# Optimization experiments

Measured on AMD Instinct MI355X. Metric: run time of the kernel, lower is better.

Reference implementation:

```python
import jax, jax.numpy as jnp
import numpy as np

B, H, W, C = 8, 128, 128, 192
HEADS, WS, SS = 6, 8, 4
MLP_H = 384  # mlp_ratio=2.0
N = WS * WS
NW = (H // WS) * (W // WS)


def _rel_index():
    coords = np.stack(np.meshgrid(np.arange(WS), np.arange(WS), indexing='ij'))  # [2,ws,ws]
    flat = coords.reshape(2, -1)
    rel = (flat[:, :, None] - flat[:, None, :]).transpose(1, 2, 0).astype(np.int64)  # [n,n,2]
    rel[..., 0] += WS - 1
    rel[..., 1] += WS - 1
    rel[..., 0] *= 2 * WS - 1
    return rel.sum(-1)  # [n,n]


def _attn_mask():
    img = np.zeros((H, W), dtype=np.float32)
    sl = (slice(0, -WS), slice(-WS, -SS), slice(-SS, None))
    cnt = 0
    for hs in sl:
        for ws_ in sl:
            img[hs, ws_] = cnt
            cnt += 1
    mw = img.reshape(H // WS, WS, W // WS, WS).transpose(0, 2, 1, 3).reshape(-1, N)
    diff = mw[:, None, :] - mw[:, :, None]  # [nW,n,n]
    return np.where(diff != 0, np.float32(-100.0), np.float32(0.0))


def setup_inputs() -> dict:
    key = jax.random.key(0)
    ks = jax.random.split(key, 6)
    rn = lambda k, shp: jax.random.normal(k, shp, jnp.float32) * 0.02
    return {
        'x': jax.random.normal(ks[0], (B, H * W, C), jnp.float32),
        'norm1_g': jnp.ones((C,), jnp.float32), 'norm1_b': jnp.zeros((C,), jnp.float32),
        'qkv_w': rn(ks[1], (3 * C, C)), 'qkv_b': jnp.zeros((3 * C,), jnp.float32),
        'rpb_table': rn(ks[2], ((2 * WS - 1) ** 2, HEADS)),
        'proj_w': rn(ks[3], (C, C)), 'proj_b': jnp.zeros((C,), jnp.float32),
        'norm2_g': jnp.ones((C,), jnp.float32), 'norm2_b': jnp.zeros((C,), jnp.float32),
        'fc1_w': rn(ks[4], (MLP_H, C)), 'fc1_b': jnp.zeros((MLP_H,), jnp.float32),
        'fc2_w': rn(ks[5], (C, MLP_H)), 'fc2_b': jnp.zeros((C,), jnp.float32),
        'rel_idx': jnp.asarray(_rel_index(), jnp.int32),
        'attn_mask': jnp.asarray(_attn_mask()),
    }


def _ln(x, g, b):
    m = x.mean(-1, keepdims=True)
    v = x.var(-1, keepdims=True)
    return (x - m) * jax.lax.rsqrt(v + 1e-5) * g + b


def _block(x, norm1_g, norm1_b, qkv_w, qkv_b, rpb_table, proj_b_w, proj_b_b,
           norm2_g, norm2_b, fc1_w, fc1_b, fc2_w, fc2_b, rel_idx, attn_mask):
    hd = C // HEADS
    scale = hd ** (-0.5)
    shortcut = x
    h = _ln(x, norm1_g, norm1_b).reshape(B, H, W, C)
    # cyclic shift
    h = jnp.roll(h, (-SS, -SS), axis=(1, 2))
    # window partition -> [B*nW, n, C]
    xw = h.reshape(B, H // WS, WS, W // WS, WS, C).transpose(0, 1, 3, 2, 4, 5).reshape(-1, N, C)
    qkv = (xw @ qkv_w.T + qkv_b).reshape(-1, N, 3, HEADS, hd).transpose(2, 0, 3, 1, 4)
    q, k, v = qkv[0] * scale, qkv[1], qkv[2]  # each [B*nW, heads, n, hd]
    attn = jnp.einsum('whnd,whmd->whnm', q, k)
    bias = rpb_table[rel_idx.reshape(-1)].reshape(N, N, HEADS).transpose(2, 0, 1)  # [heads,n,n]
    attn = attn + bias[None]
    attn = (attn.reshape(B, NW, HEADS, N, N) + attn_mask[None, :, None]).reshape(-1, HEADS, N, N)
    attn = jax.nn.softmax(attn, axis=-1)
    out = jnp.einsum('whnm,whmd->whnd', attn, v).transpose(0, 2, 1, 3).reshape(-1, N, C)
    out = out @ proj_b_w.T + proj_b_b
    # window reverse
    out = out.reshape(B, H // WS, W // WS, WS, WS, C).transpose(0, 1, 3, 2, 4, 5).reshape(B, H, W, C)
    out = jnp.roll(out, (SS, SS), axis=(1, 2)).reshape(B, H * W, C)
    x = shortcut + out
    hm = _ln(x, norm2_g, norm2_b)
    hm = jax.nn.gelu(hm @ fc1_w.T + fc1_b, approximate=False) @ fc2_w.T + fc2_b
    return x + hm


def reference(x, norm1_g, norm1_b, qkv_w, qkv_b, rpb_table, proj_w, proj_b,
              norm2_g, norm2_b, fc1_w, fc1_b, fc2_w, fc2_b, rel_idx, attn_mask):
    return _block(x, norm1_g, norm1_b, qkv_w, qkv_b, rpb_table, proj_w, proj_b,
                  norm2_g, norm2_b, fc1_w, fc1_b, fc2_w, fc2_b, rel_idx, attn_mask)
```

## Files before the change

kernel.cpp:

```cpp
#include <hip/hip_runtime.h>
#include <hip/hip_bf16.h>


typedef __hip_bfloat16 bf16;
typedef __bf16 bf16x8 __attribute__((ext_vector_type(8)));
typedef __bf16 bf16x4 __attribute__((ext_vector_type(4)));
typedef float f32x4 __attribute__((ext_vector_type(4)));

static __device__ __forceinline__ bf16x8 ldg8(const bf16* p) {
    return *reinterpret_cast<const bf16x8*>(p);
}

static __device__ __forceinline__ float gelu_f(float x) {
    float z  = x * 0.70710678118654752f;
    float az = __builtin_fabsf(z);
    float t  = __builtin_amdgcn_rcpf(__builtin_fmaf(0.3275911f, az, 1.f));
    float p  = __builtin_fmaf(1.061405429f, t, -1.453152027f);
    p = __builtin_fmaf(p, t, 1.421413741f);
    p = __builtin_fmaf(p, t, -0.284496736f);
    p = __builtin_fmaf(p, t, 0.254829592f);
    p = p * t;
    float e  = __expf(-az * az);
    float er = __builtin_fmaf(-p, e, 1.f);
    er = __builtin_copysignf(er, z);
    return 0.5f * x * (1.f + er);
}

__global__ __launch_bounds__(256) void cvt_scale_kernel(
    const float* __restrict__ src, const float* __restrict__ g,
    bf16* __restrict__ dst, int n, int K)
{
    int i = (blockIdx.x * 256 + threadIdx.x) * 4;
    if (i < n) {
        float4 v = *reinterpret_cast<const float4*>(src + i);
        int c = i % K;
        if (g) { v.x *= g[c]; v.y *= g[c + 1]; v.z *= g[c + 2]; v.w *= g[c + 3]; }
        dst[i]     = __float2bfloat16(v.x);
        dst[i + 1] = __float2bfloat16(v.y);
        dst[i + 2] = __float2bfloat16(v.z);
        dst[i + 3] = __float2bfloat16(v.w);
    }
}

__global__ __launch_bounds__(64) void bias_fold_kernel(
    const float* __restrict__ b0, const float* __restrict__ W,
    const float* __restrict__ beta, float* __restrict__ bout, int K)
{
    int f = blockIdx.x, lane = threadIdx.x;
    float s = 0.f;
    for (int c = lane; c < K; c += 64) s += beta[c] * W[(size_t)f * K + c];
#pragma unroll
    for (int off = 32; off; off >>= 1) s += __shfl_xor(s, off, 64);
    if (lane == 0) bout[f] = b0[f] + s;
}

__global__ __launch_bounds__(256) void bm_kernel(
    const float* __restrict__ rpb, const int* __restrict__ rel,
    const float* __restrict__ amask, bf16* __restrict__ bmT)
{
    int wm = blockIdx.x / 6, head = blockIdx.x % 6;
    const float* mrow = amask + (size_t)wm * 4096;
    bf16* o = bmT + (size_t)blockIdx.x * 4096;
    for (int idx = threadIdx.x; idx < 4096; idx += 256) {
        int nk = idx >> 6, nq = idx & 63;
        int t = nq * 64 + nk;
        o[idx] = __float2bfloat16(rpb[rel[t] * 6 + head] + mrow[t]);
    }
}

__global__ __launch_bounds__(256) void qkv_ln(
    const float* __restrict__ x, const bf16* __restrict__ W,
    const float* __restrict__ bias, bf16* __restrict__ q,
    bf16* __restrict__ k, bf16* __restrict__ vt)
{
    __shared__ __align__(16) bf16 xs[64][208];
    int wave = threadIdx.x >> 6, lane = threadIdx.x & 63;
    int quad = lane >> 4, l16 = lane & 15;
    int win = blockIdx.x;
    int b = win >> 8, wrem = win & 255, wr = wrem >> 4, wc = wrem & 15;

    {
        int n = wave * 16 + l16;
        int ii = n >> 3, jj = n & 7;
        int h = (wr * 8 + ii + 4) & 127, w2 = (wc * 8 + jj + 4) & 127;
        const float* xp = x + ((size_t)b * 16384 + h * 128 + w2) * 192 + quad * 8;
        float e[48];
        float sum = 0.f, sq = 0.f;
#pragma unroll
        for (int kk = 0; kk < 6; ++kk) {
            float4 u0 = *reinterpret_cast<const float4*>(xp + kk * 32);
            float4 u1 = *reinterpret_cast<const float4*>(xp + kk * 32 + 4);
            e[kk * 8 + 0] = u0.x; e[kk * 8 + 1] = u0.y; e[kk * 8 + 2] = u0.z; e[kk * 8 + 3] = u0.w;
            e[kk * 8 + 4] = u1.x; e[kk * 8 + 5] = u1.y; e[kk * 8 + 6] = u1.z; e[kk * 8 + 7] = u1.w;
#pragma unroll
            for (int j = 0; j < 8; ++j) { float v = e[kk * 8 + j]; sum += v; sq += v * v; }
        }
        sum += __shfl_xor(sum, 16, 64); sum += __shfl_xor(sum, 32, 64);
        sq  += __shfl_xor(sq, 16, 64);  sq  += __shfl_xor(sq, 32, 64);
        float mean = sum * (1.f / 192.f);
        float rstd = rsqrtf(sq * (1.f / 192.f) - mean * mean + 1e-5f);
#pragma unroll
        for (int kk = 0; kk < 6; ++kk) {
            bf16x8 pk;
#pragma unroll
            for (int j = 0; j < 8; ++j)
                pk[j] = (__bf16)((e[kk * 8 + j] - mean) * rstd);
            *reinterpret_cast<bf16x8*>(&xs[n][kk * 32 + quad * 8]) = pk;
        }
    }
    __syncthreads();
    bf16x8 a[4][6];
#pragma unroll
    for (int mt = 0; mt < 4; ++mt)
#pragma unroll
        for (int kk = 0; kk < 6; ++kk)
            a[mt][kk] = *reinterpret_cast<const bf16x8*>(&xs[mt * 16 + l16][kk * 32 + quad * 8]);

#pragma unroll 1
    for (int i = 0; i < 9; ++i) {
        int nt = wave * 9 + i;
        const bf16* wrow = W + (size_t)(nt * 16 + l16) * 192 + quad * 8;
        bf16x8 bfr[6];
#pragma unroll
        for (int kk = 0; kk < 6; ++kk) bfr[kk] = ldg8(wrow + kk * 32);
        f32x4 acc[4];
#pragma unroll
        for (int mt = 0; mt < 4; ++mt) {
            f32x4 z = {0.f, 0.f, 0.f, 0.f};
#pragma unroll
            for (int kk = 0; kk < 6; ++kk)
                z = __builtin_amdgcn_mfma_f32_16x16x32_bf16(a[mt][kk], bfr[kk], z, 0, 0, 0);
            acc[mt] = z;
        }
        int f = nt * 16 + l16;
        float bb = bias[f];
        int which = f / 192;
        int head = (f % 192) >> 5;
        int d = f & 31;
        size_t wh2 = (size_t)(win * 6 + head) * 2048;
        if (which == 2) {
#pragma unroll
            for (int mt = 0; mt < 4; ++mt) {
                bf16x4 pk;
#pragma unroll
                for (int r = 0; r < 4; ++r) pk[r] = (__bf16)(acc[mt][r] + bb);
                *reinterpret_cast<bf16x4*>(vt + wh2 + d * 64 + mt * 16 + quad * 4) = pk;
            }
        } else {
            float sc = (which == 0) ? 0.17677669529663687f : 1.f;
            bf16* dst = (which == 1) ? k : q;
#pragma unroll
            for (int mt = 0; mt < 4; ++mt)
#pragma unroll
                for (int r = 0; r < 4; ++r) {
                    int n = mt * 16 + quad * 4 + r;
                    dst[wh2 + n * 32 + d] = __float2bfloat16((acc[mt][r] + bb) * sc);
                }
        }
    }
}

__global__ __launch_bounds__(256) void attn_kernel(
    const bf16* __restrict__ q, const bf16* __restrict__ k,
    const bf16* __restrict__ vt, const bf16* __restrict__ bmT,
    bf16* __restrict__ ao)
{
    __shared__ __align__(16) bf16 lds[4][64 * 72];
    int wave = threadIdx.x >> 6, lane = threadIdx.x & 63;
    int quad = lane >> 4, l16 = lane & 15;
    int wh = blockIdx.x * 4 + wave;
    int win = wh / 6, head = wh - win * 6;
    const bf16* Qp = q + (size_t)wh * 2048;
    const bf16* Kp = k + (size_t)wh * 2048;
    const bf16* Vp = vt + (size_t)wh * 2048;
    const bf16* bm = bmT + (size_t)((win & 255) * 6 + head) * 4096;

    bf16x8 kf[4], qf[4];
#pragma unroll
    for (int t = 0; t < 4; ++t) {
        kf[t] = ldg8(Kp + (t * 16 + l16) * 32 + quad * 8);
        qf[t] = ldg8(Qp + (t * 16 + l16) * 32 + quad * 8);
    }
    f32x4 s[4][4];
#pragma unroll
    for (int mt = 0; mt < 4; ++mt)
#pragma unroll
        for (int nt = 0; nt < 4; ++nt) {
            f32x4 z = {0.f, 0.f, 0.f, 0.f};
            s[mt][nt] = __builtin_amdgcn_mfma_f32_16x16x32_bf16(kf[mt], qf[nt], z, 0, 0, 0);
        }
#pragma unroll
    for (int mt = 0; mt < 4; ++mt)
#pragma unroll
        for (int nt = 0; nt < 4; ++nt)
#pragma unroll
            for (int r = 0; r < 4; ++r) {
                int nk = mt * 16 + quad * 4 + r, nq = nt * 16 + l16;
                s[mt][nt][r] += __bfloat162float(bm[nk * 64 + nq]);
            }
    float linv[4];
#pragma unroll
    for (int nt = 0; nt < 4; ++nt) {
        float mx = -3.0e38f;
#pragma unroll
        for (int mt = 0; mt < 4; ++mt)
#pragma unroll
            for (int r = 0; r < 4; ++r) mx = fmaxf(mx, s[mt][nt][r]);
        mx = fmaxf(mx, __shfl_xor(mx, 16, 64));
        mx = fmaxf(mx, __shfl_xor(mx, 32, 64));
        float sum = 0.f;
#pragma unroll
        for (int mt = 0; mt < 4; ++mt)
#pragma unroll
            for (int r = 0; r < 4; ++r) {
                float p = __expf(s[mt][nt][r] - mx);
                s[mt][nt][r] = p;
                sum += p;
            }
        sum += __shfl_xor(sum, 16, 64);
        sum += __shfl_xor(sum, 32, 64);
        linv[nt] = 1.f / sum;
    }
    bf16* lp = lds[wave];
#pragma unroll
    for (int mt = 0; mt < 4; ++mt)
#pragma unroll
        for (int nt = 0; nt < 4; ++nt)
#pragma unroll
            for (int r = 0; r < 4; ++r)
                lp[(nt * 16 + l16) * 72 + mt * 16 + quad * 4 + r] =
                    __float2bfloat16(s[mt][nt][r] * linv[nt]);
    f32x4 o[4][2];
#pragma unroll
    for (int mo = 0; mo < 4; ++mo)
#pragma unroll
        for (int no = 0; no < 2; ++no) o[mo][no] = (f32x4){0.f, 0.f, 0.f, 0.f};
#pragma unroll
    for (int kh = 0; kh < 2; ++kh) {
        bf16x8 pf[4];
#pragma unroll
        for (int mo = 0; mo < 4; ++mo)
            pf[mo] = *reinterpret_cast<const bf16x8*>(
                lp + (mo * 16 + l16) * 72 + kh * 32 + quad * 8);
#pragma unroll
        for (int no = 0; no < 2; ++no) {
            bf16x8 vf = ldg8(Vp + (no * 16 + l16) * 64 + kh * 32 + quad * 8);
#pragma unroll
            for (int mo = 0; mo < 4; ++mo)
                o[mo][no] = __builtin_amdgcn_mfma_f32_16x16x32_bf16(pf[mo], vf, o[mo][no], 0, 0, 0);
        }
    }
    bf16* ob = ao + (size_t)wh * 2048;
#pragma unroll
    for (int mo = 0; mo < 4; ++mo)
#pragma unroll
        for (int r = 0; r < 4; ++r) {
            int nq = mo * 16 + quad * 4 + r;
            ob[nq * 32 + l16]      = __float2bfloat16(o[mo][0][r]);
            ob[nq * 32 + 16 + l16] = __float2bfloat16(o[mo][1][r]);
        }
}

__global__ __launch_bounds__(256, 3) void proj_ln(
    const bf16* __restrict__ ao, const bf16* __restrict__ W,
    const float* __restrict__ pb, const float* __restrict__ x,
    float* __restrict__ x1w, bf16* __restrict__ xn2)
{
    __shared__ float zt[64][196];
    __shared__ float part[4][64], part2[4][64], ms[64][2];
    int wave = threadIdx.x >> 6, lane = threadIdx.x & 63;
    int quad = lane >> 4, l16 = lane & 15;
    int win = blockIdx.x;
    int b = win >> 8, wrem = win & 255, wr = wrem >> 4, wc = wrem & 15;
    bf16x8 bw[3][6];
#pragma unroll
    for (int i = 0; i < 3; ++i) {
        const bf16* wp = W + (size_t)((wave * 3 + i) * 16 + l16) * 192 + quad * 8;
#pragma unroll
        for (int kk = 0; kk < 6; ++kk) bw[i][kk] = ldg8(wp + kk * 32);
    }
    f32x4 z[3][4];
#pragma unroll
    for (int mt = 0; mt < 4; ++mt) {
        bf16x8 a6[6];
#pragma unroll
        for (int h = 0; h < 6; ++h)
            a6[h] = ldg8(ao + (size_t)(win * 6 + h) * 2048 + (mt * 16 + l16) * 32 + quad * 8);
#pragma unroll
        for (int i = 0; i < 3; ++i) {
            f32x4 zz = {0.f, 0.f, 0.f, 0.f};
#pragma unroll
            for (int kk = 0; kk < 6; ++kk)
                zz = __builtin_amdgcn_mfma_f32_16x16x32_bf16(a6[kk], bw[i][kk], zz, 0, 0, 0);
            z[i][mt] = zz;
        }
    }
#pragma unroll
    for (int i = 0; i < 3; ++i) {
        int c = (wave * 3 + i) * 16 + l16;
        float bb = pb[c];
#pragma unroll
        for (int mt = 0; mt < 4; ++mt)
#pragma unroll
            for (int r = 0; r < 4; ++r) {
                int n = mt * 16 + quad * 4 + r;
                int ii = n >> 3, jj = n & 7;
                int h = (wr * 8 + ii + 4) & 127, w2 = (wc * 8 + jj + 4) & 127;
                size_t sidx = ((size_t)b * 16384 + h * 128 + w2) * 192 + c;
                float v = z[i][mt][r] + bb + x[sidx];
                z[i][mt][r] = v;
                zt[n][c] = v;
            }
    }
#pragma unroll
    for (int mt = 0; mt < 4; ++mt)
#pragma unroll
        for (int r = 0; r < 4; ++r) {
            float s1 = 0.f, s2 = 0.f;
#pragma unroll
            for (int i = 0; i < 3; ++i) {
                float v = z[i][mt][r];
                s1 += v; s2 += v * v;
            }
#pragma unroll
            for (int off = 1; off < 16; off <<= 1) {
                s1 += __shfl_xor(s1, off, 64);
                s2 += __shfl_xor(s2, off, 64);
            }
            if (l16 == 0) {
                int row = mt * 16 + quad * 4 + r;
                part[wave][row] = s1;
                part2[wave][row] = s2;
            }
        }
    __syncthreads();
    if (threadIdx.x < 64) {
        int t = threadIdx.x;
        float S = part[0][t] + part[1][t] + part[2][t] + part[3][t];
        float S2 = part2[0][t] + part2[1][t] + part2[2][t] + part2[3][t];
        float m = S * (1.f / 192.f);
        ms[t][0] = m;
        ms[t][1] = rsqrtf(S2 * (1.f / 192.f) - m * m + 1e-5f);
    }
    __syncthreads();
    int tid = threadIdx.x;
#pragma unroll 1
    for (int s = 0; s < 12; ++s) {
        int idx = s * 256 + tid;
        int row = idx / 48, c4 = idx - row * 48;
        float4 v = *reinterpret_cast<const float4*>(&zt[row][c4 * 4]);
        *reinterpret_cast<float4*>(&x1w[((size_t)win * 64 + row) * 192 + c4 * 4]) = v;
    }
#pragma unroll 1
    for (int s = 0; s < 6; ++s) {
        int idx = s * 256 + tid;
        int row = idx / 24, c8 = idx - row * 24;
        float m = ms[row][0], rs = ms[row][1];
        float4 u0 = *reinterpret_cast<const float4*>(&zt[row][c8 * 8]);
        float4 u1 = *reinterpret_cast<const float4*>(&zt[row][c8 * 8 + 4]);
        bf16x8 pk;
        pk[0] = (__bf16)((u0.x - m) * rs); pk[1] = (__bf16)((u0.y - m) * rs);
        pk[2] = (__bf16)((u0.z - m) * rs); pk[3] = (__bf16)((u0.w - m) * rs);
        pk[4] = (__bf16)((u1.x - m) * rs); pk[5] = (__bf16)((u1.y - m) * rs);
        pk[6] = (__bf16)((u1.z - m) * rs); pk[7] = (__bf16)((u1.w - m) * rs);
        *reinterpret_cast<bf16x8*>(&xn2[((size_t)win * 64 + row) * 192 + c8 * 8]) = pk;
    }
}

__global__ __launch_bounds__(256, 3) void mlp_kernel(
    const bf16* __restrict__ xn2, const bf16* __restrict__ W1,
    const float* __restrict__ b1, const bf16* __restrict__ W2,
    const float* __restrict__ b2, const float* __restrict__ x1w,
    float* __restrict__ out)
{
    __shared__ __align__(16) bf16 hsh[64 * 392];
    int wave = threadIdx.x >> 6, lane = threadIdx.x & 63;
    int quad = lane >> 4, l16 = lane & 15;
    int win = blockIdx.x;
    size_t mbase = (size_t)win * 64;
    int b = win >> 8, wrem = win & 255, wr = wrem >> 4, wc = wrem & 15;
    bf16x8 a[4][6];
#pragma unroll
    for (int mt = 0; mt < 4; ++mt) {
        const bf16* ar = xn2 + (mbase + mt * 16 + l16) * 192 + quad * 8;
#pragma unroll
        for (int kk = 0; kk < 6; ++kk) a[mt][kk] = ldg8(ar + kk * 32);
    }
#pragma unroll 1
    for (int i = 0; i < 6; ++i) {
        int nt = wave * 6 + i;
        const bf16* wp = W1 + (size_t)(nt * 16 + l16) * 192 + quad * 8;
        bf16x8 bfr[6];
#pragma unroll
        for (int kk = 0; kk < 6; ++kk) bfr[kk] = ldg8(wp + kk * 32);
        float bb = b1[nt * 16 + l16];
#pragma unroll
        for (int mt = 0; mt < 4; ++mt) {
            f32x4 zz = {0.f, 0.f, 0.f, 0.f};
#pragma unroll
            for (int kk = 0; kk < 6; ++kk)
                zz = __builtin_amdgcn_mfma_f32_16x16x32_bf16(a[mt][kk], bfr[kk], zz, 0, 0, 0);
#pragma unroll
            for (int r = 0; r < 4; ++r) {
                float gl = gelu_f(zz[r] + bb);
                hsh[(mt * 16 + quad * 4 + r) * 392 + nt * 16 + l16] = __float2bfloat16(gl);
            }
        }
    }
    __syncthreads();
#pragma unroll 1
    for (int j = 0; j < 3; ++j) {
        int c = (wave * 3 + j) * 16 + l16;
        const bf16* wp = W2 + (size_t)c * 384 + quad * 8;
        bf16x8 bw[12];
#pragma unroll
        for (int kk = 0; kk < 12; ++kk) bw[kk] = ldg8(wp + kk * 32);
        float bb = b2[c];
#pragma unroll 1
        for (int mt = 0; mt < 4; ++mt) {
            f32x4 zz = {0.f, 0.f, 0.f, 0.f};
#pragma unroll
            for (int kk = 0; kk < 12; ++kk) {
                bf16x8 pa = *reinterpret_cast<const bf16x8*>(
                    hsh + (mt * 16 + l16) * 392 + kk * 32 + quad * 8);
                zz = __builtin_amdgcn_mfma_f32_16x16x32_bf16(pa, bw[kk], zz, 0, 0, 0);
            }
#pragma unroll
            for (int r = 0; r < 4; ++r) {
                int row = mt * 16 + quad * 4 + r;
                int ii = row >> 3, jj = row & 7;
                int h = (wr * 8 + ii + 4) & 127, w2c = (wc * 8 + jj + 4) & 127;
                size_t didx = ((size_t)b * 16384 + h * 128 + w2c) * 192 + c;
                out[didx] = zz[r] + bb + x1w[(mbase + row) * 192 + c];
            }
        }
    }
}

extern "C" void kernel_launch(void* const* d_in, const int* in_sizes, int n_in,
                              void* d_out, int out_size, void* d_ws, size_t ws_size,
                              hipStream_t stream)
{
    const float* x     = (const float*)d_in[0];
    const float* n1g   = (const float*)d_in[1];
    const float* n1b   = (const float*)d_in[2];
    const float* qkvw  = (const float*)d_in[3];
    const float* qkvb  = (const float*)d_in[4];
    const float* rpb   = (const float*)d_in[5];
    const float* projw = (const float*)d_in[6];
    const float* projb = (const float*)d_in[7];
    const float* n2g   = (const float*)d_in[8];
    const float* n2b   = (const float*)d_in[9];
    const float* fc1w  = (const float*)d_in[10];
    const float* fc1b  = (const float*)d_in[11];
    const float* fc2w  = (const float*)d_in[12];
    const float* fc2b  = (const float*)d_in[13];
    const int*   rel   = (const int*)d_in[14];
    const float* amask = (const float*)d_in[15];
    float* out = (float*)d_out;

    char* ws = (char*)d_ws;
    const size_t SZ = (size_t)131072 * 192 * 2;
    bf16* qb  = (bf16*)(ws);
    bf16* kb  = (bf16*)(ws + SZ);
    bf16* vtb = (bf16*)(ws + 2 * SZ);
    bf16* aob = (bf16*)(ws + 3 * SZ);
    char* wreg = ws + 4 * SZ;
    bf16*  wq  = (bf16*)(wreg);
    bf16*  wp  = wq + 110592;
    bf16*  w1  = wp + 36864;
    bf16*  w2  = w1 + 73728;
    float* bq  = (float*)(w2 + 73728);
    float* b1  = bq + 576;
    bf16*  bmT = (bf16*)(b1 + 384);
    float* x1w = (float*)(ws);
    bf16*  xn2 = vtb;

    cvt_scale_kernel<<<108, 256, 0, stream>>>(qkvw, n1g, wq, 110592, 192);
    cvt_scale_kernel<<<36, 256, 0, stream>>>(projw, nullptr, wp, 36864, 192);
    cvt_scale_kernel<<<72, 256, 0, stream>>>(fc1w, n2g, w1, 73728, 192);
    cvt_scale_kernel<<<72, 256, 0, stream>>>(fc2w, nullptr, w2, 73728, 384);
    bias_fold_kernel<<<576, 64, 0, stream>>>(qkvb, qkvw, n1b, bq, 192);
    bias_fold_kernel<<<384, 64, 0, stream>>>(fc1b, fc1w, n2b, b1, 192);
    bm_kernel<<<1536, 256, 0, stream>>>(rpb, rel, amask, bmT);
    qkv_ln<<<2048, 256, 0, stream>>>(x, wq, bq, qb, kb, vtb);
    attn_kernel<<<3072, 256, 0, stream>>>(qb, kb, vtb, bmT, aob);
    proj_ln<<<2048, 256, 0, stream>>>(aob, wp, projb, x, x1w, xn2);
    mlp_kernel<<<2048, 256, 0, stream>>>(xn2, w1, b1, w2, fc2b, x1w, out);
}
```

Measured before the change: 542.3 us.

## Fuse projection+LayerNorm kernel with MLP kernel to keep residual on-chip

Merges the proj_ln and mlp_kernel launches into a single proj_mlp kernel per window. The post-attention residual stays in registers and the normalized activations go through shared memory instead of being written to and reread from global workspace buffers (x1w fp32 and xn2 bf16). This removes one launch and a large global round-trip. In exchange, register and LDS pressure rise, since the z accumulators live across the MLP and there is an extra shared buffer, and occupancy is lowered to 2 blocks per SM.

```diff
diff --git a/kernel.cpp b/kernel.cpp
--- a/kernel.cpp
+++ b/kernel.cpp
@@ -261,38 +261,44 @@
         }
 }
 
-__global__ __launch_bounds__(256, 3) void proj_ln(
-    const bf16* __restrict__ ao, const bf16* __restrict__ W,
+__global__ __launch_bounds__(256, 2) void proj_mlp(
+    const bf16* __restrict__ ao, const bf16* __restrict__ Wp,
     const float* __restrict__ pb, const float* __restrict__ x,
-    float* __restrict__ x1w, bf16* __restrict__ xn2)
-{
-    __shared__ float zt[64][196];
+    const bf16* __restrict__ W1, const float* __restrict__ b1,
+    const bf16* __restrict__ W2, const float* __restrict__ b2,
+    float* __restrict__ out)
+{
+    __shared__ __align__(16) bf16 hsh[64 * 392];
+    __shared__ __align__(16) bf16 xsn[64 * 200];
     __shared__ float part[4][64], part2[4][64], ms[64][2];
     int wave = threadIdx.x >> 6, lane = threadIdx.x & 63;
     int quad = lane >> 4, l16 = lane & 15;
     int win = blockIdx.x;
     int b = win >> 8, wrem = win & 255, wr = wrem >> 4, wc = wrem & 15;
-    bf16x8 bw[3][6];
-#pragma unroll
-    for (int i = 0; i < 3; ++i) {
-        const bf16* wp = W + (size_t)((wave * 3 + i) * 16 + l16) * 192 + quad * 8;
-#pragma unroll
-        for (int kk = 0; kk < 6; ++kk) bw[i][kk] = ldg8(wp + kk * 32);
-    }
+
     f32x4 z[3][4];
-#pragma unroll
-    for (int mt = 0; mt < 4; ++mt) {
-        bf16x8 a6[6];
-#pragma unroll
-        for (int h = 0; h < 6; ++h)
-            a6[h] = ldg8(ao + (size_t)(win * 6 + h) * 2048 + (mt * 16 + l16) * 32 + quad * 8);
+    {
+        bf16x8 bw[3][6];
 #pragma unroll
         for (int i = 0; i < 3; ++i) {
-            f32x4 zz = {0.f, 0.f, 0.f, 0.f};
-#pragma unroll
-            for (int kk = 0; kk < 6; ++kk)
-                zz = __builtin_amdgcn_mfma_f32_16x16x32_bf16(a6[kk], bw[i][kk], zz, 0, 0, 0);
-            z[i][mt] = zz;
+            const bf16* wp = Wp + (size_t)((wave * 3 + i) * 16 + l16) * 192 + quad * 8;
+#pragma unroll
+            for (int kk = 0; kk < 6; ++kk) bw[i][kk] = ldg8(wp + kk * 32);
+        }
+#pragma unroll
+        for (int mt = 0; mt < 4; ++mt) {
+            bf16x8 a6[6];
+#pragma unroll
+            for (int h = 0; h < 6; ++h)
+                a6[h] = ldg8(ao + (size_t)(win * 6 + h) * 2048 + (mt * 16 + l16) * 32 + quad * 8);
+#pragma unroll
+            for (int i = 0; i < 3; ++i) {
+                f32x4 zz = {0.f, 0.f, 0.f, 0.f};
+#pragma unroll
+                for (int kk = 0; kk < 6; ++kk)
+                    zz = __builtin_amdgcn_mfma_f32_16x16x32_bf16(a6[kk], bw[i][kk], zz, 0, 0, 0);
+                z[i][mt] = zz;
+            }
         }
     }
 #pragma unroll
@@ -307,9 +313,7 @@
                 int ii = n >> 3, jj = n & 7;
                 int h = (wr * 8 + ii + 4) & 127, w2 = (wc * 8 + jj + 4) & 127;
                 size_t sidx = ((size_t)b * 16384 + h * 128 + w2) * 192 + c;
-                float v = z[i][mt][r] + bb + x[sidx];
-                z[i][mt][r] = v;
-                zt[n][c] = v;
+                z[i][mt][r] += bb + x[sidx];
             }
     }
 #pragma unroll
@@ -343,72 +347,51 @@
         ms[t][1] = rsqrtf(S2 * (1.f / 192.f) - m * m + 1e-5f);
     }
     __syncthreads();
-    int tid = threadIdx.x;
+#pragma unroll
+    for (int i = 0; i < 3; ++i) {
+        int c = (wave * 3 + i) * 16 + l16;
+#pragma unroll
+        for (int mt = 0; mt < 4; ++mt)
+#pragma unroll
+            for (int r = 0; r < 4; ++r) {
+                int row = mt * 16 + quad * 4 + r;
+                xsn[row * 200 + c] =
+                    __float2bfloat16((z[i][mt][r] - ms[row][0]) * ms[row][1]);
+            }
+    }
+    __syncthreads();
+    {
+        bf16x8 a[4][6];
+#pragma unroll
+        for (int mt = 0; mt < 4; ++mt)
+#pragma unroll
+            for (int kk = 0; kk < 6; ++kk)
+                a[mt][kk] = *reinterpret_cast<const bf16x8*>(
+                    &xsn[(mt * 16 + l16) * 200 + kk * 32 + quad * 8]);
 #pragma unroll 1
-    for (int s = 0; s < 12; ++s) {
-        int idx = s * 256 + tid;
-        int row = idx / 48, c4 = idx - row * 48;
-        float4 v = *reinterpret_cast<const float4*>(&zt[row][c4 * 4]);
-        *reinterpret_cast<float4*>(&x1w[((size_t)win * 64 + row) * 192 + c4 * 4]) = v;
-    }
-#pragma unroll 1
-    for (int s = 0; s < 6; ++s) {
-        int idx = s * 256 + tid;
-        int row = idx / 24, c8 = idx - row * 24;
-        float m = ms[row][0], rs = ms[row][1];
-        float4 u0 = *reinterpret_cast<const float4*>(&zt[row][c8 * 8]);
-        float4 u1 = *reinterpret_cast<const float4*>(&zt[row][c8 * 8 + 4]);
-        bf16x8 pk;
-        pk[0] = (__bf16)((u0.x - m) * rs); pk[1] = (__bf16)((u0.y - m) * rs);
-        pk[2] = (__bf16)((u0.z - m) * rs); pk[3] = (__bf16)((u0.w - m) * rs);
-        pk[4] = (__bf16)((u1.x - m) * rs); pk[5] = (__bf16)((u1.y - m) * rs);
-        pk[6] = (__bf16)((u1.z - m) * rs); pk[7] = (__bf16)((u1.w - m) * rs);
-        *reinterpret_cast<bf16x8*>(&xn2[((size_t)win * 64 + row) * 192 + c8 * 8]) = pk;
-    }
-}
-
-__global__ __launch_bounds__(256, 3) void mlp_kernel(
-    const bf16* __restrict__ xn2, const bf16* __restrict__ W1,
-    const float* __restrict__ b1, const bf16* __restrict__ W2,
-    const float* __restrict__ b2, const float* __restrict__ x1w,
-    float* __restrict__ out)
-{
-    __shared__ __align__(16) bf16 hsh[64 * 392];
-    int wave = threadIdx.x >> 6, lane = threadIdx.x & 63;
-    int quad = lane >> 4, l16 = lane & 15;
-    int win = blockIdx.x;
-    size_t mbase = (size_t)win * 64;
-    int b = win >> 8, wrem = win & 255, wr = wrem >> 4, wc = wrem & 15;
-    bf16x8 a[4][6];
-#pragma unroll
-    for (int mt = 0; mt < 4; ++mt) {
-        const bf16* ar = xn2 + (mbase + mt * 16 + l16) * 192 + quad * 8;
-#pragma unroll
-        for (int kk = 0; kk < 6; ++kk) a[mt][kk] = ldg8(ar + kk * 32);
-    }
-#pragma unroll 1
-    for (int i = 0; i < 6; ++i) {
-        int nt = wave * 6 + i;
-        const bf16* wp = W1 + (size_t)(nt * 16 + l16) * 192 + quad * 8;
-        bf16x8 bfr[6];
-#pragma unroll
-        for (int kk = 0; kk < 6; ++kk) bfr[kk] = ldg8(wp + kk * 32);
-        float bb = b1[nt * 16 + l16];
-#pragma unroll
-        for (int mt = 0; mt < 4; ++mt) {
-            f32x4 zz = {0.f, 0.f, 0.f, 0.f};
-#pragma unroll
-            for (int kk = 0; kk < 6; ++kk)
-                zz = __builtin_amdgcn_mfma_f32_16x16x32_bf16(a[mt][kk], bfr[kk], zz, 0, 0, 0);
-#pragma unroll
-            for (int r = 0; r < 4; ++r) {
-                float gl = gelu_f(zz[r] + bb);
-                hsh[(mt * 16 + quad * 4 + r) * 392 + nt * 16 + l16] = __float2bfloat16(gl);
+        for (int i = 0; i < 6; ++i) {
+            int nt = wave * 6 + i;
+            const bf16* wp = W1 + (size_t)(nt * 16 + l16) * 192 + quad * 8;
+            bf16x8 bfr[6];
+#pragma unroll
+            for (int kk = 0; kk < 6; ++kk) bfr[kk] = ldg8(wp + kk * 32);
+            float bb = b1[nt * 16 + l16];
+#pragma unroll
+            for (int mt = 0; mt < 4; ++mt) {
+                f32x4 zz = {0.f, 0.f, 0.f, 0.f};
+#pragma unroll
+                for (int kk = 0; kk < 6; ++kk)
+                    zz = __builtin_amdgcn_mfma_f32_16x16x32_bf16(a[mt][kk], bfr[kk], zz, 0, 0, 0);
+#pragma unroll
+                for (int r = 0; r < 4; ++r) {
+                    float gl = gelu_f(zz[r] + bb);
+                    hsh[(mt * 16 + quad * 4 + r) * 392 + nt * 16 + l16] = __float2bfloat16(gl);
+                }
             }
         }
     }
     __syncthreads();
-#pragma unroll 1
+#pragma unroll
     for (int j = 0; j < 3; ++j) {
         int c = (wave * 3 + j) * 16 + l16;
         const bf16* wp = W2 + (size_t)c * 384 + quad * 8;
@@ -422,7 +405,7 @@
 #pragma unroll
             for (int kk = 0; kk < 12; ++kk) {
                 bf16x8 pa = *reinterpret_cast<const bf16x8*>(
-                    hsh + (mt * 16 + l16) * 392 + kk * 32 + quad * 8);
+                    &hsh[(mt * 16 + l16) * 392 + kk * 32 + quad * 8]);
                 zz = __builtin_amdgcn_mfma_f32_16x16x32_bf16(pa, bw[kk], zz, 0, 0, 0);
             }
 #pragma unroll
@@ -431,7 +414,7 @@
                 int ii = row >> 3, jj = row & 7;
                 int h = (wr * 8 + ii + 4) & 127, w2c = (wc * 8 + jj + 4) & 127;
                 size_t didx = ((size_t)b * 16384 + h * 128 + w2c) * 192 + c;
-                out[didx] = zz[r] + bb + x1w[(mbase + row) * 192 + c];
+                out[didx] = zz[r] + bb + z[j][mt][r];
             }
         }
     }
@@ -473,8 +456,6 @@
     float* bq  = (float*)(w2 + 73728);
     float* b1  = bq + 576;
     bf16*  bmT = (bf16*)(b1 + 384);
-    float* x1w = (float*)(ws);
-    bf16*  xn2 = vtb;
 
     cvt_scale_kernel<<<108, 256, 0, stream>>>(qkvw, n1g, wq, 110592, 192);
     cvt_scale_kernel<<<36, 256, 0, stream>>>(projw, nullptr, wp, 36864, 192);
@@ -485,6 +466,5 @@
     bm_kernel<<<1536, 256, 0, stream>>>(rpb, rel, amask, bmT);
     qkv_ln<<<2048, 256, 0, stream>>>(x, wq, bq, qb, kb, vtb);
     attn_kernel<<<3072, 256, 0, stream>>>(qb, kb, vtb, bmT, aob);
-    proj_ln<<<2048, 256, 0, stream>>>(aob, wp, projb, x, x1w, xn2);
-    mlp_kernel<<<2048, 256, 0, stream>>>(xn2, w1, b1, w2, fc2b, x1w, out);
-}
+    proj_mlp<<<2048, 256, 0, stream>>>(aob, wp, projb, x, w1, b1, w2, fc2b, out);
+}
```

Result: faster. 529.5 us (-2.4%).
